# Performance work log

Measured on AMD Instinct MI355X. Metric: run time of the kernel, lower is better.

Reference implementation:

```python
import jax, jax.numpy as jnp
import numpy as np


def setup_inputs() -> dict:
    key = jax.random.key(0)
    k1, k2 = jax.random.split(key)
    B, H, W, C = 8, 2048, 2048, 21
    yp = jax.random.randint(k1, (B, H, W), 0, C, dtype=jnp.int32)
    y = jax.random.randint(k2, (B, H, W), 0, C, dtype=jnp.int32)
    res = jnp.zeros((B, C, C), dtype=jnp.float32)
    return {"yp": yp, "y": y, "res": res, "n_classes": C}


def reference(yp, y, res, n_classes):
    # Faithful math of Confusion_Matrix.forward:
    # res[i] = histogram over pixels of (yp*n_classes + y), reshaped [C, C].
    # (The torch scatter trick sets x2[i][idx_j, j] = 1 on a zero buffer and
    #  sums over j -> exactly a bincount of idx; res input is fully overwritten.)
    B = yp.shape[0]
    C = n_classes
    idx = (yp.reshape(B, -1) * C + y.reshape(B, -1))  # [B, N] int32 in [0, C*C)
    hist = jnp.zeros((B, C * C), dtype=jnp.float32)
    hist = hist.at[jnp.arange(B)[:, None], idx].add(1.0)
    return hist.reshape(B, C, C)
```

## Files before the change

kernel.cpp:

```cpp
#include <hip/hip_runtime.h>

constexpr int C    = 21;
constexpr int CC   = C * C;
constexpr int NSUB = 8;

__global__ __launch_bounds__(256, 8)
void conf_hist(const int* __restrict__ yp,
               const int* __restrict__ y,
               float* __restrict__ out,
               int n_per_batch,
               int blocks_per_batch) {
    __shared__ unsigned int hist[NSUB][CC];

    const int tid = threadIdx.x;
    for (int i = tid; i < (NSUB * CC) / 4; i += 256)
        ((uint4*)hist)[i] = make_uint4(0u, 0u, 0u, 0u);
    __syncthreads();

    const int b   = blockIdx.x / blocks_per_batch;
    const int blk = blockIdx.x - b * blocks_per_batch;

    const int4* yp4 = (const int4*)(yp + (size_t)b * n_per_batch);
    const int4* y4  = (const int4*)(y  + (size_t)b * n_per_batch);
    const int n4     = n_per_batch >> 2;
    const int stride = blocks_per_batch * 256;

    unsigned int* h = hist[tid >> 5];

    int i = blk * 256 + tid;

    for (; i + 3 * stride < n4; i += 4 * stride) {
        int4 a0 = yp4[i];
        int4 a1 = yp4[i + stride];
        int4 a2 = yp4[i + 2 * stride];
        int4 a3 = yp4[i + 3 * stride];
        int4 c0 = y4[i];
        int4 c1 = y4[i + stride];
        int4 c2 = y4[i + 2 * stride];
        int4 c3 = y4[i + 3 * stride];
        __builtin_amdgcn_sched_barrier(0);

        atomicAdd(&h[a0.x * C + c0.x], 1u);
        atomicAdd(&h[a0.y * C + c0.y], 1u);
        atomicAdd(&h[a0.z * C + c0.z], 1u);
        atomicAdd(&h[a0.w * C + c0.w], 1u);
        atomicAdd(&h[a1.x * C + c1.x], 1u);
        atomicAdd(&h[a1.y * C + c1.y], 1u);
        atomicAdd(&h[a1.z * C + c1.z], 1u);
        atomicAdd(&h[a1.w * C + c1.w], 1u);
        atomicAdd(&h[a2.x * C + c2.x], 1u);
        atomicAdd(&h[a2.y * C + c2.y], 1u);
        atomicAdd(&h[a2.z * C + c2.z], 1u);
        atomicAdd(&h[a2.w * C + c2.w], 1u);
        atomicAdd(&h[a3.x * C + c3.x], 1u);
        atomicAdd(&h[a3.y * C + c3.y], 1u);
        atomicAdd(&h[a3.z * C + c3.z], 1u);
        atomicAdd(&h[a3.w * C + c3.w], 1u);
    }
    for (; i < n4; i += stride) {
        int4 a = yp4[i];
        int4 c = y4[i];
        atomicAdd(&h[a.x * C + c.x], 1u);
        atomicAdd(&h[a.y * C + c.y], 1u);
        atomicAdd(&h[a.z * C + c.z], 1u);
        atomicAdd(&h[a.w * C + c.w], 1u);
    }
    __syncthreads();

    float* ob = out + (size_t)b * CC;
    for (int j = tid; j < CC; j += 256) {
        unsigned int s = 0;
        #pragma unroll
        for (int k = 0; k < NSUB; ++k) s += hist[k][j];
        if (s) atomicAdd(&ob[j], (float)s);
    }
}

extern "C" void kernel_launch(void* const* d_in, const int* in_sizes, int n_in,
                              void* d_out, int out_size, void* d_ws, size_t ws_size,
                              hipStream_t stream) {
    const int* yp = (const int*)d_in[0];
    const int* y  = (const int*)d_in[1];
    float* out    = (float*)d_out;

    const int total = in_sizes[0];
    const int B = out_size / CC;
    const int n_per_batch = total / B;

    hipMemsetAsync(out, 0, (size_t)out_size * sizeof(float), stream);

    const int blocks_per_batch = 256;
    conf_hist<<<B * blocks_per_batch, 256, 0, stream>>>(
        yp, y, out, n_per_batch, blocks_per_batch);
}
```

Before: 52.07 us.

## Replace global float atomics with per-block partial histograms and a finalize kernel

Each block now writes its reduced 441-bin histogram to a workspace buffer with padded stride instead of doing global float atomicAdds. A second kernel then sums the partials per batch and writes the output directly, so the memset is no longer needed. This is meant to remove contention on global atomics, at the cost of an extra kernel launch and a few MB of workspace traffic. It also drops the sched_barrier in the main loop, and when the workspace is too small it falls back to a simpler atomic kernel without the 4x unrolled load loop.

```diff
diff --git a/kernel.cpp b/kernel.cpp
--- a/kernel.cpp
+++ b/kernel.cpp
@@ -2,14 +2,15 @@
 
 constexpr int C    = 21;
 constexpr int CC   = C * C;
+constexpr int CCP  = 448;
 constexpr int NSUB = 8;
 
 __global__ __launch_bounds__(256, 8)
-void conf_hist(const int* __restrict__ yp,
-               const int* __restrict__ y,
-               float* __restrict__ out,
-               int n_per_batch,
-               int blocks_per_batch) {
+void conf_hist_partial(const int* __restrict__ yp,
+                       const int* __restrict__ y,
+                       unsigned int* __restrict__ partial,
+                       int n_per_batch,
+                       int blocks_per_batch) {
     __shared__ unsigned int hist[NSUB][CC];
 
     const int tid = threadIdx.x;
@@ -28,7 +29,6 @@
     unsigned int* h = hist[tid >> 5];
 
     int i = blk * 256 + tid;
-
     for (; i + 3 * stride < n4; i += 4 * stride) {
         int4 a0 = yp4[i];
         int4 a1 = yp4[i + stride];
@@ -38,7 +38,6 @@
         int4 c1 = y4[i + stride];
         int4 c2 = y4[i + 2 * stride];
         int4 c3 = y4[i + 3 * stride];
-        __builtin_amdgcn_sched_barrier(0);
 
         atomicAdd(&h[a0.x * C + c0.x], 1u);
         atomicAdd(&h[a0.y * C + c0.y], 1u);
@@ -58,6 +57,70 @@
         atomicAdd(&h[a3.w * C + c3.w], 1u);
     }
     for (; i < n4; i += stride) {
+        int4 a = yp4[i];
+        int4 c = y4[i];
+        atomicAdd(&h[a.x * C + c.x], 1u);
+        atomicAdd(&h[a.y * C + c.y], 1u);
+        atomicAdd(&h[a.z * C + c.z], 1u);
+        atomicAdd(&h[a.w * C + c.w], 1u);
+    }
+    __syncthreads();
+
+    unsigned int* pb = partial + (size_t)blockIdx.x * CCP;
+    for (int j = tid; j < CC; j += 256) {
+        unsigned int s = 0;
+        #pragma unroll
+        for (int k = 0; k < NSUB; ++k) s += hist[k][j];
+        pb[j] = s;
+    }
+}
+
+__global__ __launch_bounds__(256)
+void conf_finalize(const unsigned int* __restrict__ partial,
+                   float* __restrict__ out,
+                   int blocks_per_batch) {
+    const int b    = blockIdx.x / 7;
+    const int g    = blockIdx.x % 7;
+    const int lane = threadIdx.x & 63;
+    const int row0 = threadIdx.x >> 6;
+    const int bin  = g * 64 + lane;
+
+    const unsigned int* p = partial + (size_t)b * blocks_per_batch * CCP + bin;
+    unsigned int acc = 0;
+    #pragma unroll 8
+    for (int r = row0; r < blocks_per_batch; r += 4)
+        acc += p[(size_t)r * CCP];
+
+    __shared__ unsigned int sm[4][64];
+    sm[row0][lane] = acc;
+    __syncthreads();
+
+    if (threadIdx.x < 64) {
+        unsigned int s = sm[0][lane] + sm[1][lane] + sm[2][lane] + sm[3][lane];
+        if (bin < CC) out[(size_t)b * CC + bin] = (float)s;
+    }
+}
+
+__global__ __launch_bounds__(256, 8)
+void conf_hist_atomic(const int* __restrict__ yp,
+                      const int* __restrict__ y,
+                      float* __restrict__ out,
+                      int n_per_batch,
+                      int blocks_per_batch) {
+    __shared__ unsigned int hist[NSUB][CC];
+    const int tid = threadIdx.x;
+    for (int i = tid; i < (NSUB * CC) / 4; i += 256)
+        ((uint4*)hist)[i] = make_uint4(0u, 0u, 0u, 0u);
+    __syncthreads();
+
+    const int b   = blockIdx.x / blocks_per_batch;
+    const int blk = blockIdx.x - b * blocks_per_batch;
+    const int4* yp4 = (const int4*)(yp + (size_t)b * n_per_batch);
+    const int4* y4  = (const int4*)(y  + (size_t)b * n_per_batch);
+    const int n4 = n_per_batch >> 2;
+    unsigned int* h = hist[tid >> 5];
+
+    for (int i = blk * 256 + tid; i < n4; i += blocks_per_batch * 256) {
         int4 a = yp4[i];
         int4 c = y4[i];
         atomicAdd(&h[a.x * C + c.x], 1u);
@@ -87,9 +150,18 @@
     const int B = out_size / CC;
     const int n_per_batch = total / B;
 
-    hipMemsetAsync(out, 0, (size_t)out_size * sizeof(float), stream);
+    const int blocks_per_batch = 256;
+    const int nblocks = B * blocks_per_batch;
+    const size_t ws_needed = (size_t)nblocks * CCP * sizeof(unsigned int);
 
-    const int blocks_per_batch = 256;
-    conf_hist<<<B * blocks_per_batch, 256, 0, stream>>>(
-        yp, y, out, n_per_batch, blocks_per_batch);
+    if (ws_size >= ws_needed) {
+        unsigned int* partial = (unsigned int*)d_ws;
+        conf_hist_partial<<<nblocks, 256, 0, stream>>>(
+            yp, y, partial, n_per_batch, blocks_per_batch);
+        conf_finalize<<<B * 7, 256, 0, stream>>>(partial, out, blocks_per_batch);
+    } else {
+        hipMemsetAsync(out, 0, (size_t)out_size * sizeof(float), stream);
+        conf_hist_atomic<<<nblocks, 256, 0, stream>>>(
+            yp, y, out, n_per_batch, blocks_per_batch);
+    }
 }
```

New measurement: 48.74 us. 6.4% less time.
